# Kernel optimization log

Measured on AMD Instinct MI355X. Metric: run time of the kernel, lower is better.

## Reference

```python
import jax, jax.numpy as jnp
import numpy as np

B, N, M = 256, 512, 1024  # batch, out_features, in_features
TAU = 1.0


def setup_inputs() -> dict:
    key = jax.random.key(0)
    k_in, k_logits, k_gumbel = jax.random.split(key, 3)
    x = jax.random.normal(k_in, (B, M), dtype=jnp.float32)
    # kaiming_uniform_(a=sqrt(5)) on [out, in] -> bound = sqrt(6/((1+5)*fan_in)) = 1/sqrt(fan_in)
    bound = 1.0 / np.sqrt(M)
    logits = jax.random.uniform(k_logits, (N, M), dtype=jnp.float32,
                                minval=-bound, maxval=bound)
    # gumbel noise for every (batch, out, in) entry, matching the repeated logits tensor
    gumbel_noise = jax.random.gumbel(k_gumbel, (B, N, M), dtype=jnp.float32)
    return {"input": x, "logits": logits, "gumbel_noise": gumbel_noise}


def reference(input, logits, gumbel_noise):
    # soft gumbel-softmax over the in_features axis, per (batch, out) row
    z = (logits[None, :, :] + gumbel_noise) / TAU      # [B, N, M]
    w = jax.nn.softmax(z, axis=-1)                      # [B, N, M]
    # y[b, n] = sum_m w[b, n, m] * input[b, m]
    return jnp.einsum('bnm,bm->bn', w, input)           # [B, N]
```

## Files before the change

### kernel.cpp

```cpp
#include <hip/hip_runtime.h>

#define GSM_B 256
#define GSM_N 512
#define GSM_M 1024

#define ROWS_PER_WAVE 4
#define WAVES_PER_BLOCK 4
#define ROWS_PER_BLOCK (ROWS_PER_WAVE * WAVES_PER_BLOCK)

typedef __attribute__((ext_vector_type(4))) float f32x4;

__global__ __launch_bounds__(256) void gsm_rowsoftmax_dot_kernel(
    const float* __restrict__ x,
    const float* __restrict__ logits,
    const float* __restrict__ g,
    float* __restrict__ out)
{
    const int wave = threadIdx.x >> 6;
    const int lane = threadIdx.x & 63;
    const int row0 = blockIdx.x * ROWS_PER_BLOCK + wave * ROWS_PER_WAVE;
    const int b    = row0 >> 9;
    const int n0   = row0 & (GSM_N - 1);

    const f32x4* __restrict__ xv = reinterpret_cast<const f32x4*>(x + (size_t)b * GSM_M);
    f32x4 xs[4];
    #pragma unroll
    for (int j = 0; j < 4; ++j)
        xs[j] = xv[j * 64 + lane];

    float s0[ROWS_PER_WAVE];
    float s1[ROWS_PER_WAVE];

    #pragma unroll
    for (int r = 0; r < ROWS_PER_WAVE; ++r) {
        const f32x4* __restrict__ gv =
            reinterpret_cast<const f32x4*>(g + (size_t)(row0 + r) * GSM_M);
        const f32x4* __restrict__ lv =
            reinterpret_cast<const f32x4*>(logits + (size_t)(n0 + r) * GSM_M);

        float a0 = 0.0f, a1 = 0.0f;
        #pragma unroll
        for (int j = 0; j < 4; ++j) {
            const int idx4 = j * 64 + lane;
            const f32x4 gg = __builtin_nontemporal_load(&gv[idx4]);
            const f32x4 ll = lv[idx4];
            const float e0 = __expf(ll.x + gg.x);
            const float e1 = __expf(ll.y + gg.y);
            const float e2 = __expf(ll.z + gg.z);
            const float e3 = __expf(ll.w + gg.w);
            a0 += (e0 + e1) + (e2 + e3);
            a1 += (e0 * xs[j].x + e1 * xs[j].y) + (e2 * xs[j].z + e3 * xs[j].w);
        }
        s0[r] = a0;
        s1[r] = a1;
    }

    #pragma unroll
    for (int off = 1; off < 64; off <<= 1) {
        float t0[ROWS_PER_WAVE], t1[ROWS_PER_WAVE];
        #pragma unroll
        for (int r = 0; r < ROWS_PER_WAVE; ++r) {
            t0[r] = __shfl_xor(s0[r], off, 64);
            t1[r] = __shfl_xor(s1[r], off, 64);
        }
        #pragma unroll
        for (int r = 0; r < ROWS_PER_WAVE; ++r) {
            s0[r] += t0[r];
            s1[r] += t1[r];
        }
    }

    if (lane == 0) {
        f32x4 res;
        res.x = s1[0] / s0[0];
        res.y = s1[1] / s0[1];
        res.z = s1[2] / s0[2];
        res.w = s1[3] / s0[3];
        *reinterpret_cast<f32x4*>(out + row0) = res;
    }
}

extern "C" void kernel_launch(void* const* d_in, const int* in_sizes, int n_in,
                              void* d_out, int out_size, void* d_ws, size_t ws_size,
                              hipStream_t stream) {
    const float* x      = (const float*)d_in[0];
    const float* logits = (const float*)d_in[1];
    const float* g      = (const float*)d_in[2];
    float* out          = (float*)d_out;

    const int rows   = GSM_B * GSM_N;
    const int blocks = rows / ROWS_PER_BLOCK;
    gsm_rowsoftmax_dot_kernel<<<blocks, 256, 0, stream>>>(x, logits, g, out);
}
```

Baseline: 655.7 us.

## Prescale logits by log2e, use exp2 with FMA, and double-buffer row loads

Adds a small prep kernel that writes logits scaled by log2(e) into workspace. The main kernel then computes exp2(g*log2e + lp) with one FMA and the native exp2 instead of add plus __expf. It also prefetches the next row's gumbel and logit vectors while computing the current row, and sets an occupancy hint in launch bounds. This costs an extra kernel launch and a 2 MB write and read, and the double buffer raises register pressure. The workload is dominated by streaming the 512 MB gumbel tensor, so gains are likely small.

```diff
diff --git a/kernel.cpp b/kernel.cpp
--- a/kernel.cpp
+++ b/kernel.cpp
@@ -8,9 +8,118 @@
 #define WAVES_PER_BLOCK 4
 #define ROWS_PER_BLOCK (ROWS_PER_WAVE * WAVES_PER_BLOCK)
 
+#define LOG2E 1.44269504088896340736f
+
 typedef __attribute__((ext_vector_type(4))) float f32x4;
 
-__global__ __launch_bounds__(256) void gsm_rowsoftmax_dot_kernel(
+__global__ __launch_bounds__(256) void gsm_prep_lp(
+    const float* __restrict__ logits, float* __restrict__ lp)
+{
+    const int i = blockIdx.x * 256 + threadIdx.x;
+    f32x4 v = reinterpret_cast<const f32x4*>(logits)[i];
+    f32x4 o;
+    o.x = v.x * LOG2E;
+    o.y = v.y * LOG2E;
+    o.z = v.z * LOG2E;
+    o.w = v.w * LOG2E;
+    reinterpret_cast<f32x4*>(lp)[i] = o;
+}
+
+__global__ __launch_bounds__(256, 4) void gsm_rowsoftmax_dot_kernel(
+    const float* __restrict__ x,
+    const float* __restrict__ lp,
+    const float* __restrict__ g,
+    float* __restrict__ out)
+{
+    const int wave = threadIdx.x >> 6;
+    const int lane = threadIdx.x & 63;
+    const int row0 = blockIdx.x * ROWS_PER_BLOCK + wave * ROWS_PER_WAVE;
+    const int b    = row0 >> 9;
+    const int n0   = row0 & (GSM_N - 1);
+
+    const f32x4* __restrict__ xv = reinterpret_cast<const f32x4*>(x + (size_t)b * GSM_M);
+    f32x4 xs[4];
+    #pragma unroll
+    for (int j = 0; j < 4; ++j)
+        xs[j] = xv[j * 64 + lane];
+
+    f32x4 gbuf[2][4], lbuf[2][4];
+
+    {
+        const f32x4* __restrict__ gv =
+            reinterpret_cast<const f32x4*>(g + (size_t)row0 * GSM_M);
+        const f32x4* __restrict__ lv =
+            reinterpret_cast<const f32x4*>(lp + (size_t)n0 * GSM_M);
+        #pragma unroll
+        for (int j = 0; j < 4; ++j) {
+            gbuf[0][j] = __builtin_nontemporal_load(&gv[j * 64 + lane]);
+            lbuf[0][j] = lv[j * 64 + lane];
+        }
+    }
+
+    float s0[ROWS_PER_WAVE];
+    float s1[ROWS_PER_WAVE];
+
+    #pragma unroll
+    for (int r = 0; r < ROWS_PER_WAVE; ++r) {
+        if (r + 1 < ROWS_PER_WAVE) {
+            const f32x4* __restrict__ gv =
+                reinterpret_cast<const f32x4*>(g + (size_t)(row0 + r + 1) * GSM_M);
+            const f32x4* __restrict__ lv =
+                reinterpret_cast<const f32x4*>(lp + (size_t)(n0 + r + 1) * GSM_M);
+            #pragma unroll
+            for (int j = 0; j < 4; ++j) {
+                gbuf[(r + 1) & 1][j] = __builtin_nontemporal_load(&gv[j * 64 + lane]);
+                lbuf[(r + 1) & 1][j] = lv[j * 64 + lane];
+            }
+        }
+
+        float a0 = 0.0f, a1 = 0.0f;
+        #pragma unroll
+        for (int j = 0; j < 4; ++j) {
+            const f32x4 gg = gbuf[r & 1][j];
+            const f32x4 ll = lbuf[r & 1][j];
+            const float z0 = __builtin_fmaf(gg.x, LOG2E, ll.x);
+            const float z1 = __builtin_fmaf(gg.y, LOG2E, ll.y);
+            const float z2 = __builtin_fmaf(gg.z, LOG2E, ll.z);
+            const float z3 = __builtin_fmaf(gg.w, LOG2E, ll.w);
+            const float e0 = __builtin_amdgcn_exp2f(z0);
+            const float e1 = __builtin_amdgcn_exp2f(z1);
+            const float e2 = __builtin_amdgcn_exp2f(z2);
+            const float e3 = __builtin_amdgcn_exp2f(z3);
+            a0 += (e0 + e1) + (e2 + e3);
+            a1 += (e0 * xs[j].x + e1 * xs[j].y) + (e2 * xs[j].z + e3 * xs[j].w);
+        }
+        s0[r] = a0;
+        s1[r] = a1;
+    }
+
+    #pragma unroll
+    for (int off = 1; off < 64; off <<= 1) {
+        float t0[ROWS_PER_WAVE], t1[ROWS_PER_WAVE];
+        #pragma unroll
+        for (int r = 0; r < ROWS_PER_WAVE; ++r) {
+            t0[r] = __shfl_xor(s0[r], off, 64);
+            t1[r] = __shfl_xor(s1[r], off, 64);
+        }
+        #pragma unroll
+        for (int r = 0; r < ROWS_PER_WAVE; ++r) {
+            s0[r] += t0[r];
+            s1[r] += t1[r];
+        }
+    }
+
+    if (lane == 0) {
+        f32x4 res;
+        res.x = s1[0] / s0[0];
+        res.y = s1[1] / s0[1];
+        res.z = s1[2] / s0[2];
+        res.w = s1[3] / s0[3];
+        *reinterpret_cast<f32x4*>(out + row0) = res;
+    }
+}
+
+__global__ __launch_bounds__(256, 4) void gsm_rowsoftmax_dot_kernel_raw(
     const float* __restrict__ x,
     const float* __restrict__ logits,
     const float* __restrict__ g,
@@ -28,8 +137,7 @@
     for (int j = 0; j < 4; ++j)
         xs[j] = xv[j * 64 + lane];
 
-    float s0[ROWS_PER_WAVE];
-    float s1[ROWS_PER_WAVE];
+    float s0[ROWS_PER_WAVE], s1[ROWS_PER_WAVE];
 
     #pragma unroll
     for (int r = 0; r < ROWS_PER_WAVE; ++r) {
@@ -37,7 +145,6 @@
             reinterpret_cast<const f32x4*>(g + (size_t)(row0 + r) * GSM_M);
         const f32x4* __restrict__ lv =
             reinterpret_cast<const f32x4*>(logits + (size_t)(n0 + r) * GSM_M);
-
         float a0 = 0.0f, a1 = 0.0f;
         #pragma unroll
         for (int j = 0; j < 4; ++j) {
@@ -90,5 +197,13 @@
 
     const int rows   = GSM_B * GSM_N;
     const int blocks = rows / ROWS_PER_BLOCK;
-    gsm_rowsoftmax_dot_kernel<<<blocks, 256, 0, stream>>>(x, logits, g, out);
-}
+
+    const size_t lp_bytes = (size_t)GSM_N * GSM_M * sizeof(float);
+    if (d_ws != nullptr && ws_size >= lp_bytes) {
+        float* lp = (float*)d_ws;
+        gsm_prep_lp<<<(GSM_N * GSM_M / 4) / 256, 256, 0, stream>>>(logits, lp);
+        gsm_rowsoftmax_dot_kernel<<<blocks, 256, 0, stream>>>(x, lp, g, out);
+    } else {
+        gsm_rowsoftmax_dot_kernel_raw<<<blocks, 256, 0, stream>>>(x, logits, g, out);
+    }
+}
```

After: 661.0 us. Within noise of the previous version (+0.8%).
